# Kernel tuning notes

Hardware: AMD Instinct MI355X
Metric: run time of the kernel (lower is better)

Reference implementation:

```python
import jax, jax.numpy as jnp
import numpy as np

# Segmented tensor product, uniform-1d case (subscripts 'u,u,u'):
#   out[z, idx_out[p]*u:(idx_out[p]+1)*u] += coeffs[p] * x0_seg[z, idx0[p]] * x1_seg[z, idx1[p]]
U = 128          # mode extent 'u'
NSEG = (32, 8, 32)  # segments per operand (in0, in1, out)
P = 128          # number of paths
Z = 16384        # batch


def setup_inputs() -> dict:
    key = jax.random.key(0)
    k0, k1, k2, k3, k4, k5 = jax.random.split(key, 6)
    return {
        "x0": jax.random.normal(k0, (Z, NSEG[0] * U), dtype=jnp.float32),
        "x1": jax.random.normal(k1, (Z, NSEG[1] * U), dtype=jnp.float32),
        "coeffs": jax.random.normal(k2, (P,), dtype=jnp.float32),
        "idx0": jax.random.randint(k3, (P,), 0, NSEG[0], dtype=jnp.int32),
        "idx1": jax.random.randint(k4, (P,), 0, NSEG[1], dtype=jnp.int32),
        "idx_out": jax.random.randint(k5, (P,), 0, NSEG[2], dtype=jnp.int32),
    }


def reference(x0, x1, coeffs, idx0, idx1, idx_out):
    z = x0.shape[0]
    x0r = x0.reshape(z, NSEG[0], U)  # [Z, n0, u]
    x1r = x1.reshape(z, NSEG[1], U)  # [Z, n1, u]
    # gather the segment used by each path: [Z, P, u]
    s0 = x0r[:, idx0, :]
    s1 = x1r[:, idx1, :]
    # per-path contribution, elementwise over u (coefficient subscript is scalar)
    contrib = (s0 * s1) * coeffs[None, :, None]          # [Z, P, u]
    # scatter-add paths into output segments
    contrib = jnp.transpose(contrib, (1, 0, 2))          # [P, Z, u]
    out_seg = jax.ops.segment_sum(contrib, idx_out, num_segments=NSEG[2])  # [n2, Z, u]
    return jnp.transpose(out_seg, (1, 0, 2)).reshape(z, NSEG[2] * U)
```

## Files before the change

kernel.cpp:

```cpp
#include <hip/hip_runtime.h>


#define Z_DIM 16384
#define U_DIM 128
#define NSEG0 32
#define NSEG1 8
#define NSEG2 32
#define P_DIM 128
#define ZPB   2
#define BLK   512

__global__ __launch_bounds__(128) void tp_setup(
    const float* __restrict__ coeffs,
    const int* __restrict__ idx0,
    const int* __restrict__ idx1,
    const int* __restrict__ idx_out,
    int* __restrict__ off_g,
    int2* __restrict__ meta_g)
{
    __shared__ int s_cnt[NSEG2];
    __shared__ int s_off[NSEG2 + 1];
    const int t = threadIdx.x;
    if (t < NSEG2) s_cnt[t] = 0;
    __syncthreads();
    const int o = idx_out[t];
    const int r = atomicAdd(&s_cnt[o], 1);
    __syncthreads();
    if (t == 0) {
        int sum = 0;
        for (int i = 0; i < NSEG2; ++i) { s_off[i] = sum; sum += s_cnt[i]; }
        s_off[NSEG2] = sum;
    }
    __syncthreads();
    meta_g[s_off[o] + r] = make_int2(idx0[t] | (idx1[t] << 16), __float_as_int(coeffs[t]));
    if (t <= NSEG2) off_g[t] = s_off[t];
}

__global__ __launch_bounds__(BLK) void tp_kernel(
    const float* __restrict__ x0,
    const float* __restrict__ x1,
    const int* __restrict__ off_g,
    const int2* __restrict__ meta_g,
    float* __restrict__ out)
{
    __shared__ float s_x0[ZPB][NSEG0 * U_DIM];
    __shared__ float s_x1[ZPB][NSEG1 * U_DIM];

    const int t = threadIdx.x;
    const size_t z0 = (size_t)blockIdx.x * ZPB;

    {
        const float4* g0 = reinterpret_cast<const float4*>(x0 + z0 * (NSEG0 * U_DIM));
        const float4* g1 = reinterpret_cast<const float4*>(x1 + z0 * (NSEG1 * U_DIM));
        float4* l0 = reinterpret_cast<float4*>(&s_x0[0][0]);
        float4* l1 = reinterpret_cast<float4*>(&s_x1[0][0]);
#if __has_builtin(__builtin_amdgcn_global_load_lds)
        #pragma unroll
        for (int i = 0; i < (ZPB * NSEG0 * U_DIM / 4) / BLK; ++i)
            __builtin_amdgcn_global_load_lds(
                (const __attribute__((address_space(1))) void*)(g0 + i * BLK + t),
                (__attribute__((address_space(3))) void*)(l0 + i * BLK + t),
                16, 0, 0);
        __builtin_amdgcn_global_load_lds(
            (const __attribute__((address_space(1))) void*)(g1 + t),
            (__attribute__((address_space(3))) void*)(l1 + t),
            16, 0, 0);
#else
        #pragma unroll
        for (int i = 0; i < (ZPB * NSEG0 * U_DIM / 4) / BLK; ++i)
            l0[i * BLK + t] = g0[i * BLK + t];
        l1[t] = g1[t];
#endif
    }
    __syncthreads();

    const int w4 = __builtin_amdgcn_readfirstlane(t >> 6) * 4;
    const int zl = (t >> 5) & 1;
    const int uq = t & 31;

    const float* x0base = &s_x0[zl][uq * 4];
    const float* x1base = &s_x1[zl][uq * 4];
    const size_t z = z0 + zl;
    float4* orow = reinterpret_cast<float4*>(out + z * (NSEG2 * U_DIM)) + uq;

    #pragma unroll
    for (int oo = 0; oo < 4; ++oo) {
        const int o = w4 + oo;
        const int b = off_g[o];
        const int e = off_g[o + 1];
        float4 acc = make_float4(0.f, 0.f, 0.f, 0.f);
        for (int k = b; k < e; ++k) {
            const int2  m = meta_g[k];
            const float c = __int_as_float(m.y);
            const float4 a = *reinterpret_cast<const float4*>(x0base + (m.x & 0xffff) * U_DIM);
            const float4 v = *reinterpret_cast<const float4*>(x1base + (m.x >> 16)    * U_DIM);
            acc.x = fmaf(c, a.x * v.x, acc.x);
            acc.y = fmaf(c, a.y * v.y, acc.y);
            acc.z = fmaf(c, a.z * v.z, acc.z);
            acc.w = fmaf(c, a.w * v.w, acc.w);
        }
        orow[o * (U_DIM / 4)] = acc;
    }
}

extern "C" void kernel_launch(void* const* d_in, const int* in_sizes, int n_in,
                              void* d_out, int out_size, void* d_ws, size_t ws_size,
                              hipStream_t stream) {
    const float* x0      = (const float*)d_in[0];
    const float* x1      = (const float*)d_in[1];
    const float* coeffs  = (const float*)d_in[2];
    const int*   idx0    = (const int*)d_in[3];
    const int*   idx1    = (const int*)d_in[4];
    const int*   idx_out = (const int*)d_in[5];
    float* out = (float*)d_out;

    int*  off_g  = (int*)d_ws;
    int2* meta_g = (int2*)((char*)d_ws + 256);

    tp_setup<<<1, P_DIM, 0, stream>>>(coeffs, idx0, idx1, idx_out, off_g, meta_g);
    tp_kernel<<<Z_DIM / ZPB, BLK, 0, stream>>>(x0, x1, off_g, meta_g, out);
}
```

Baseline: 118.0 us.

## Make the tensor-product kernel persistent with double-buffered LDS prefetch

The main kernel now launches a fixed 512 blocks, each walking 16 batch tiles in a loop. It uses two LDS buffers so the direct global-to-LDS load of the next tile runs while the current tile is computed. The setup kernel precomputes byte offsets for the segment indices, which drops the multiply in the inner loop, and outputs are written with nontemporal stores. In exchange, the doubled LDS footprint cuts resident blocks per CU, and the prefetch is only guaranteed complete at the next barrier. Since the kernel is already close to memory bandwidth, the room for gains is limited.

```diff
diff --git a/kernel.cpp b/kernel.cpp
--- a/kernel.cpp
+++ b/kernel.cpp
@@ -9,6 +9,15 @@
 #define P_DIM 128
 #define ZPB   2
 #define BLK   512
+#define NBLOCKS 512
+#define NTILES  (Z_DIM / ZPB)
+#define TILES_PER_BLOCK (NTILES / NBLOCKS)
+
+#define X0_FLOATS (ZPB * NSEG0 * U_DIM)
+#define X1_FLOATS (ZPB * NSEG1 * U_DIM)
+#define BUF_FLOATS (X0_FLOATS + X1_FLOATS)
+
+typedef float f32x4 __attribute__((ext_vector_type(4)));
 
 __global__ __launch_bounds__(128) void tp_setup(
     const float* __restrict__ coeffs,
@@ -32,8 +41,29 @@
         s_off[NSEG2] = sum;
     }
     __syncthreads();
-    meta_g[s_off[o] + r] = make_int2(idx0[t] | (idx1[t] << 16), __float_as_int(coeffs[t]));
+    meta_g[s_off[o] + r] = make_int2((idx0[t] * (U_DIM * 4)) | ((idx1[t] * (U_DIM * 4)) << 16),
+                                     __float_as_int(coeffs[t]));
     if (t <= NSEG2) off_g[t] = s_off[t];
+}
+
+__device__ __forceinline__ void stage_tile(const float* __restrict__ x0,
+                                           const float* __restrict__ x1,
+                                           float* lbuf, size_t z0, int t)
+{
+    const float4* g0 = reinterpret_cast<const float4*>(x0 + z0 * (NSEG0 * U_DIM));
+    const float4* g1 = reinterpret_cast<const float4*>(x1 + z0 * (NSEG1 * U_DIM));
+    float4* l0 = reinterpret_cast<float4*>(lbuf);
+    float4* l1 = reinterpret_cast<float4*>(lbuf + X0_FLOATS);
+    #pragma unroll
+    for (int i = 0; i < (X0_FLOATS / 4) / BLK; ++i)
+        __builtin_amdgcn_global_load_lds(
+            (const __attribute__((address_space(1))) void*)(g0 + i * BLK + t),
+            (__attribute__((address_space(3))) void*)(l0 + i * BLK + t),
+            16, 0, 0);
+    __builtin_amdgcn_global_load_lds(
+        (const __attribute__((address_space(1))) void*)(g1 + t),
+        (__attribute__((address_space(3))) void*)(l1 + t),
+        16, 0, 0);
 }
 
 __global__ __launch_bounds__(BLK) void tp_kernel(
@@ -43,63 +73,47 @@
     const int2* __restrict__ meta_g,
     float* __restrict__ out)
 {
-    __shared__ float s_x0[ZPB][NSEG0 * U_DIM];
-    __shared__ float s_x1[ZPB][NSEG1 * U_DIM];
+    __shared__ float buf[2][BUF_FLOATS];
 
-    const int t = threadIdx.x;
-    const size_t z0 = (size_t)blockIdx.x * ZPB;
-
-    {
-        const float4* g0 = reinterpret_cast<const float4*>(x0 + z0 * (NSEG0 * U_DIM));
-        const float4* g1 = reinterpret_cast<const float4*>(x1 + z0 * (NSEG1 * U_DIM));
-        float4* l0 = reinterpret_cast<float4*>(&s_x0[0][0]);
-        float4* l1 = reinterpret_cast<float4*>(&s_x1[0][0]);
-#if __has_builtin(__builtin_amdgcn_global_load_lds)
-        #pragma unroll
-        for (int i = 0; i < (ZPB * NSEG0 * U_DIM / 4) / BLK; ++i)
-            __builtin_amdgcn_global_load_lds(
-                (const __attribute__((address_space(1))) void*)(g0 + i * BLK + t),
-                (__attribute__((address_space(3))) void*)(l0 + i * BLK + t),
-                16, 0, 0);
-        __builtin_amdgcn_global_load_lds(
-            (const __attribute__((address_space(1))) void*)(g1 + t),
-            (__attribute__((address_space(3))) void*)(l1 + t),
-            16, 0, 0);
-#else
-        #pragma unroll
-        for (int i = 0; i < (ZPB * NSEG0 * U_DIM / 4) / BLK; ++i)
-            l0[i * BLK + t] = g0[i * BLK + t];
-        l1[t] = g1[t];
-#endif
-    }
-    __syncthreads();
-
+    const int t  = threadIdx.x;
     const int w4 = __builtin_amdgcn_readfirstlane(t >> 6) * 4;
     const int zl = (t >> 5) & 1;
     const int uq = t & 31;
 
-    const float* x0base = &s_x0[zl][uq * 4];
-    const float* x1base = &s_x1[zl][uq * 4];
-    const size_t z = z0 + zl;
-    float4* orow = reinterpret_cast<float4*>(out + z * (NSEG2 * U_DIM)) + uq;
+    const size_t tile0 = (size_t)blockIdx.x * TILES_PER_BLOCK;
 
-    #pragma unroll
-    for (int oo = 0; oo < 4; ++oo) {
-        const int o = w4 + oo;
-        const int b = off_g[o];
-        const int e = off_g[o + 1];
-        float4 acc = make_float4(0.f, 0.f, 0.f, 0.f);
-        for (int k = b; k < e; ++k) {
-            const int2  m = meta_g[k];
-            const float c = __int_as_float(m.y);
-            const float4 a = *reinterpret_cast<const float4*>(x0base + (m.x & 0xffff) * U_DIM);
-            const float4 v = *reinterpret_cast<const float4*>(x1base + (m.x >> 16)    * U_DIM);
-            acc.x = fmaf(c, a.x * v.x, acc.x);
-            acc.y = fmaf(c, a.y * v.y, acc.y);
-            acc.z = fmaf(c, a.z * v.z, acc.z);
-            acc.w = fmaf(c, a.w * v.w, acc.w);
+    stage_tile(x0, x1, &buf[0][0], tile0 * ZPB, t);
+
+    int cur = 0;
+    for (int i = 0; i < TILES_PER_BLOCK; ++i) {
+        __syncthreads();
+
+        if (i + 1 < TILES_PER_BLOCK)
+            stage_tile(x0, x1, &buf[cur ^ 1][0], (tile0 + i + 1) * ZPB, t);
+
+        const float* x0base = &buf[cur][zl * (NSEG0 * U_DIM) + uq * 4];
+        const float* x1base = &buf[cur][X0_FLOATS + zl * (NSEG1 * U_DIM) + uq * 4];
+        const size_t z = (tile0 + i) * ZPB + zl;
+        float* orow = out + z * (NSEG2 * U_DIM) + uq * 4;
+
+        #pragma unroll
+        for (int oo = 0; oo < 4; ++oo) {
+            const int o = w4 + oo;
+            const int b = off_g[o];
+            const int e = off_g[o + 1];
+            f32x4 acc = (f32x4)0.f;
+            for (int k = b; k < e; ++k) {
+                const int2  m = meta_g[k];
+                const float c = __int_as_float(m.y);
+                const f32x4 a = *reinterpret_cast<const f32x4*>(
+                    reinterpret_cast<const char*>(x0base) + (m.x & 0xffff));
+                const f32x4 v = *reinterpret_cast<const f32x4*>(
+                    reinterpret_cast<const char*>(x1base) + ((unsigned)m.x >> 16));
+                acc += a * v * c;
+            }
+            __builtin_nontemporal_store(acc, reinterpret_cast<f32x4*>(orow + o * U_DIM));
         }
-        orow[o * (U_DIM / 4)] = acc;
+        cur ^= 1;
     }
 }
 
@@ -118,5 +132,5 @@
     int2* meta_g = (int2*)((char*)d_ws + 256);
 
     tp_setup<<<1, P_DIM, 0, stream>>>(coeffs, idx0, idx1, idx_out, off_g, meta_g);
-    tp_kernel<<<Z_DIM / ZPB, BLK, 0, stream>>>(x0, x1, off_g, meta_g, out);
+    tp_kernel<<<NBLOCKS, BLK, 0, stream>>>(x0, x1, off_g, meta_g, out);
 }
```

After: 122.7 us. 1.04x slower.
